# Kernel optimization log

Measured on AMD Instinct MI355X. Metric: run time of the kernel, lower is better.

## Reference

```python
import jax, jax.numpy as jnp
import numpy as np

N = 50000      # nodes
E = 800000     # edges
D = 128        # input_dim = nb_hidden = emb_dim
A = 4          # nb_edge_types (edge attr dim)
H = 2          # heads (MyGATConv default)
G = 128        # number of graphs (g.batch)
NEG = 0.2      # leaky_relu negative slope
L = 3          # nb_layers


def _glorot(key, shape):
    lim = np.sqrt(6.0 / (shape[-2] + shape[-1]))
    return jax.random.uniform(key, shape, minval=-lim, maxval=lim, dtype=jnp.float32)


def setup_inputs():
    key = jax.random.key(0)
    ks = jax.random.split(key, 20)
    inp = {
        "x": jax.random.normal(ks[0], (N, D), jnp.float32),
        "edge_index": jax.random.randint(ks[1], (2, E), 0, N, dtype=jnp.int32),
        "edge_attr": jax.random.normal(ks[2], (E, A), jnp.float32),
        "batch": jnp.sort(jax.random.randint(ks[3], (N,), 0, G, dtype=jnp.int32)),
    }
    for l in range(L):
        inp[f"linN{l}"] = _glorot(ks[4 + 4 * l], (D, H * D))
        inp[f"linE{l}"] = _glorot(ks[5 + 4 * l], (A, H * A))
        inp[f"att{l}"] = _glorot(ks[6 + 4 * l], (1, H, 2 * D + A))
        inp[f"bias{l}"] = jnp.zeros((H * D,), jnp.float32)
    inp["fw"] = _glorot(ks[16], (D, 1))
    inp["fb"] = jnp.zeros((1,), jnp.float32)
    return inp


def _gat_layer(x_in, e_in, src, dst, linN, linE, att, bias):
    n = x_in.shape[0]
    x = (x_in @ linN + bias).reshape(n, H, D)              # [N,H,D]
    e = (e_in @ linE).reshape(-1, H, A)                    # [E,H,A]
    # alpha = (cat([x_i, x_j, e], -1) * att).sum(-1); x_i = x[src], x_j = x[dst]
    ai = jnp.einsum('nhc,hc->nh', x, att[0, :, :D])        # per-node, gathered at src
    aj = jnp.einsum('nhc,hc->nh', x, att[0, :, D:2 * D])   # per-node, gathered at dst
    ae = jnp.einsum('ehc,hc->eh', e, att[0, :, 2 * D:])
    alpha = jax.nn.leaky_relu(ai[src] + aj[dst] + ae, NEG)  # [E,H]
    # segment softmax over targets (edge_index[1])
    amax = jax.ops.segment_max(alpha, dst, num_segments=n)
    ex = jnp.exp(alpha - amax[dst])
    denom = jax.ops.segment_sum(ex, dst, num_segments=n)
    alpha = ex / denom[dst]
    # PyG propagate: message = alpha * x[src], scatter-add at dst
    msg = alpha[:, :, None] * x[src]                       # [E,H,D]
    out = jax.ops.segment_sum(msg, dst, num_segments=n) + x
    # concat=False -> mean over heads, then ReLU
    return jax.nn.relu(out.mean(axis=1)), jax.nn.relu(e.mean(axis=1))


def reference(x, edge_index, edge_attr, batch,
              linN0, linE0, att0, bias0,
              linN1, linE1, att1, bias1,
              linN2, linE2, att2, bias2,
              fw, fb):
    src, dst = edge_index[0], edge_index[1]
    params = [(linN0, linE0, att0, bias0),
              (linN1, linE1, att1, bias1),
              (linN2, linE2, att2, bias2)]
    h, e = x, edge_attr
    for (lN, lE, at, b) in params:
        h, e = _gat_layer(h, e, src, dst, lN, lE, at, b)
    pooled = jax.ops.segment_sum(h, batch, num_segments=G)  # global_add_pool -> [G,D]
    y = (pooled @ fw + fb).squeeze(-1)                      # [G]
    return y
```

## Files before the change

### kernel.cpp

```cpp
#include <hip/hip_runtime.h>
#include <hip/hip_bf16.h>

#define DD 128
#define AA 4
#define HH 2

typedef short short8 __attribute__((ext_vector_type(8)));
typedef float f32x4 __attribute__((ext_vector_type(4)));

__device__ inline unsigned short f2bf(float f) {
    unsigned u = __float_as_uint(f);
    unsigned r = (u + 0x7fffu + ((u >> 16) & 1u)) >> 16;
    return (unsigned short)r;
}
__device__ inline float4 unpack_bf16x4(uint2 v) {
    float4 r;
    r.x = __uint_as_float(v.x << 16);
    r.y = __uint_as_float(v.x & 0xffff0000u);
    r.z = __uint_as_float(v.y << 16);
    r.w = __uint_as_float(v.y & 0xffff0000u);
    return r;
}
__device__ inline uint2 pack_bf16x4(float a, float b, float c, float d) {
    uint2 p;
    p.x = (unsigned)f2bf(a) | ((unsigned)f2bf(b) << 16);
    p.y = (unsigned)f2bf(c) | ((unsigned)f2bf(d) << 16);
    return p;
}


__global__ void hist_kernel(const int* __restrict__ dst, int* __restrict__ cnt, int E) {
    int e = blockIdx.x * blockDim.x + threadIdx.x;
    if (e < E) atomicAdd(&cnt[dst[e]], 1);
}

__global__ __launch_bounds__(256) void scan1(const int* __restrict__ cnt,
                                             int* __restrict__ bsum, int N) {
    __shared__ int wsh[4];
    int b = blockIdx.x, t = threadIdx.x;
    int lane = t & 63, w = t >> 6;
    int base = b * 1024;
    int v = 0;
    #pragma unroll
    for (int i = 0; i < 4; ++i) {
        int idx = base + i * 256 + t;
        v += (idx < N) ? cnt[idx] : 0;
    }
    #pragma unroll
    for (int o = 32; o; o >>= 1) v += __shfl_xor(v, o);
    if (lane == 0) wsh[w] = v;
    __syncthreads();
    if (t == 0) bsum[b] = wsh[0] + wsh[1] + wsh[2] + wsh[3];
}

__global__ __launch_bounds__(64) void scan2(int* __restrict__ bsum, int NB,
                                            int* __restrict__ total) {
    int t = threadIdx.x;
    int v = (t < NB) ? bsum[t] : 0;
    int x = v;
    #pragma unroll
    for (int o = 1; o < 64; o <<= 1) {
        int u = __shfl_up(x, o);
        if (t >= o) x += u;
    }
    if (t < NB) bsum[t] = x - v;
    if (t == 63) *total = x;
}

__global__ __launch_bounds__(256) void scan3(const int* __restrict__ cnt,
                                             const int* __restrict__ bsum,
                                             int* __restrict__ row_off,
                                             int* __restrict__ cursor, int N) {
    __shared__ int wtot[4];
    __shared__ int carry;
    int b = blockIdx.x, t = threadIdx.x;
    int lane = t & 63, w = t >> 6;
    if (t == 0) carry = bsum[b];
    __syncthreads();
    int base = b * 1024;
    #pragma unroll
    for (int it = 0; it < 4; ++it) {
        int idx = base + it * 256 + t;
        int v = (idx < N) ? cnt[idx] : 0;
        int x = v;
        #pragma unroll
        for (int o = 1; o < 64; o <<= 1) {
            int u = __shfl_up(x, o);
            if (lane >= o) x += u;
        }
        if (lane == 63) wtot[w] = x;
        __syncthreads();
        int woff = 0;
        for (int i = 0; i < w; ++i) woff += wtot[i];
        int c = carry;
        __syncthreads();
        if (t == 255) carry = c + woff + x;
        int ex = c + woff + x - v;
        if (idx < N) { row_off[idx] = ex; cursor[idx] = ex; }
        __syncthreads();
    }
}

__global__ void scatter_kernel(const int* __restrict__ src, const int* __restrict__ dst,
                               int* __restrict__ cursor, int* __restrict__ csr_src,
                               int* __restrict__ pos_of_edge, int E) {
    int e = blockIdx.x * blockDim.x + threadIdx.x;
    if (e >= E) return;
    int p = atomicAdd(&cursor[dst[e]], 1);
    csr_src[p] = src[e];
    pos_of_edge[e] = p;
}


__global__ __launch_bounds__(256) void pack_a0(const float* __restrict__ X,
                                               uint2* __restrict__ As, int N) {
    int t = blockIdx.x * blockDim.x + threadIdx.x;
    if (t >= N * 32) return;
    int r = t >> 5, kq4 = t & 31;
    float4 v = ((const float4*)X)[t];
    int g = r >> 4, m = r & 15;
    int ks = kq4 >> 3, q = (kq4 >> 1) & 3;
    int cell = ((g * 4 + ks) * 4 + q) * 16 + m;
    As[cell * 2 + (kq4 & 1)] = pack_bf16x4(v.x, v.y, v.z, v.w);
}

__global__ __launch_bounds__(256) void pack_w3(const float* __restrict__ W0,
                                               const float* __restrict__ W1,
                                               const float* __restrict__ W2,
                                               unsigned short* __restrict__ Bs) {
    int t = blockIdx.x * blockDim.x + threadIdx.x;
    if (t >= 3 * 128 * 64) return;
    int l = t / (128 * 64);
    int r = t - l * (128 * 64);
    const float* W = (l == 0) ? W0 : (l == 1) ? W1 : W2;
    unsigned short* B = Bs + (size_t)l * 128 * 256;
    int k = r >> 6, c4g = r & 63;
    float4 v = ((const float4*)W)[r];
    int ct = c4g >> 2, n0 = (c4g & 3) * 4;
    int ks = k >> 5, q = (k >> 3) & 3, j = k & 7;
    int cellbase = ((ct * 4 + ks) * 4 + q) * 16 + n0;
    B[(cellbase + 0) * 8 + j] = f2bf(v.x);
    B[(cellbase + 1) * 8 + j] = f2bf(v.y);
    B[(cellbase + 2) * 8 + j] = f2bf(v.z);
    B[(cellbase + 3) * 8 + j] = f2bf(v.w);
}


__global__ __launch_bounds__(256) void gemm_mfma(const short8* __restrict__ As,
                                                 const short8* __restrict__ Bs,
                                                 const float* __restrict__ bias,
                                                 const float* __restrict__ att,
                                                 uint2* __restrict__ xhb,
                                                 float* __restrict__ aiaj, int Ngroups) {
    __shared__ __align__(16) unsigned short sh[4][16 * 260];
    int w = threadIdx.x >> 6;
    int wid = blockIdx.x * 4 + w;
    int lane = threadIdx.x & 63;
    bool active = wid < Ngroups;
    int q = lane >> 4, m = lane & 15;

    if (active) {
        const short8* Ag = As + (size_t)wid * 256;
        f32x4 acc[16];
        #pragma unroll
        for (int ct = 0; ct < 16; ++ct) acc[ct] = (f32x4){0.f, 0.f, 0.f, 0.f};

        #pragma unroll
        for (int ks = 0; ks < 4; ++ks) {
            short8 a = Ag[ks * 64 + lane];
            #pragma unroll
            for (int ct = 0; ct < 16; ++ct) {
                short8 b = Bs[ct * 256 + ks * 64 + lane];
                acc[ct] = __builtin_amdgcn_mfma_f32_16x16x32_bf16(a, b, acc[ct], 0, 0, 0);
            }
        }

        float ai0[4] = {}, ai1[4] = {}, aj0[4] = {}, aj1[4] = {};
        #pragma unroll
        for (int ct = 0; ct < 16; ++ct) {
            int cbase = (ct & 7) * 16 + m;
            const float* atth = att + (ct >= 8 ? (2 * DD + AA) : 0);
            float aS = atth[cbase];
            float aD = atth[DD + cbase];
            float bv = bias[ct * 16 + m];
            #pragma unroll
            for (int reg = 0; reg < 4; ++reg) {
                float val = acc[ct][reg] + bv;
                sh[w][(q * 4 + reg) * 260 + ct * 16 + m] = f2bf(val);
                if (ct < 8) { ai0[reg] += val * aS; aj0[reg] += val * aD; }
                else        { ai1[reg] += val * aS; aj1[reg] += val * aD; }
            }
        }
        #pragma unroll
        for (int o = 1; o < 16; o <<= 1) {
            #pragma unroll
            for (int reg = 0; reg < 4; ++reg) {
                ai0[reg] += __shfl_xor(ai0[reg], o);
                ai1[reg] += __shfl_xor(ai1[reg], o);
                aj0[reg] += __shfl_xor(aj0[reg], o);
                aj1[reg] += __shfl_xor(aj1[reg], o);
            }
        }
        if (m == 0) {
            #pragma unroll
            for (int reg = 0; reg < 4; ++reg) {
                float4 r;
                r.x = ai0[reg]; r.y = ai1[reg]; r.z = aj0[reg]; r.w = aj1[reg];
                ((float4*)aiaj)[wid * 16 + q * 4 + reg] = r;
            }
        }
    }
    __syncthreads();
    if (active) {
        #pragma unroll
        for (int lr = 0; lr < 16; ++lr) {
            uint2 v = *(const uint2*)&sh[w][lr * 260 + lane * 4];
            xhb[(size_t)(wid * 16 + lr) * 64 + lane] = v;
        }
    }
}


__device__ inline void edge_stage(const float4& ev, const float* __restrict__ linE,
                                  const float* __restrict__ att, float2& ae, float4& enext) {
    float eh[8];
    #pragma unroll
    for (int c = 0; c < 8; ++c)
        eh[c] = ev.x * linE[c] + ev.y * linE[8 + c] + ev.z * linE[16 + c] + ev.w * linE[24 + c];
    float a0 = 0.f, a1 = 0.f;
    #pragma unroll
    for (int a = 0; a < 4; ++a) {
        a0 += eh[a]     * att[2 * DD + a];
        a1 += eh[4 + a] * att[(2 * DD + AA) + 2 * DD + a];
    }
    ae.x = a0; ae.y = a1;
    enext.x = fmaxf(0.5f * (eh[0] + eh[4]), 0.f);
    enext.y = fmaxf(0.5f * (eh[1] + eh[5]), 0.f);
    enext.z = fmaxf(0.5f * (eh[2] + eh[6]), 0.f);
    enext.w = fmaxf(0.5f * (eh[3] + eh[7]), 0.f);
}

__global__ __launch_bounds__(256) void edge_all(const float* __restrict__ ein,
                                                const float* __restrict__ linE0, const float* __restrict__ att0,
                                                const float* __restrict__ linE1, const float* __restrict__ att1,
                                                const float* __restrict__ linE2, const float* __restrict__ att2,
                                                const int* __restrict__ pos_of_edge,
                                                float2* __restrict__ ae0,
                                                float2* __restrict__ ae1,
                                                float2* __restrict__ ae2, int E) {
    int e = blockIdx.x * blockDim.x + threadIdx.x;
    if (e >= E) return;
    int p = pos_of_edge[e];
    float4 ev = ((const float4*)ein)[e];
    float2 ae; float4 en;
    edge_stage(ev, linE0, att0, ae, en); ae0[p] = ae;
    edge_stage(en, linE1, att1, ae, ev); ae1[p] = ae;
    edge_stage(ev, linE2, att2, ae, en); ae2[p] = ae;
}


__global__ __launch_bounds__(64) void aggregate(const uint2* __restrict__ xhb,
                                                const float* __restrict__ aiaj,
                                                const float2* __restrict__ ae,
                                                const int* __restrict__ row_off,
                                                const int* __restrict__ csr_src,
                                                uint2* __restrict__ hshuf,
                                                const float* __restrict__ fw,
                                                float* __restrict__ pdots, int N) {
    int d = blockIdx.x;
    int lane = threadIdx.x;
    int s0 = row_off[d], s1 = row_off[d + 1];
    int deg = s1 - s0;
    const float2* aiaj2 = (const float2*)aiaj;
    float2 ajv = aiaj2[d * 2 + 1];

    __shared__ float lex[64][2];
    __shared__ int lsrc[64];
    float4 acc = {0.f, 0.f, 0.f, 0.f};
    float den0 = 0.f, den1 = 0.f;
    int head = lane >> 5;

    for (int c = 0; c < deg; c += 64) {
        int n = min(64, deg - c);
        if (lane < n) {
            int p = s0 + c + lane;
            int s = csr_src[p];
            float2 aiv = aiaj2[s * 2];
            float2 aev = ae[p];
            float a0 = aiv.x + ajv.x + aev.x; a0 = a0 > 0.f ? a0 : 0.2f * a0;
            float a1 = aiv.y + ajv.y + aev.y; a1 = a1 > 0.f ? a1 : 0.2f * a1;
            float e0 = __expf(a0), e1 = __expf(a1);
            den0 += e0; den1 += e1;
            lex[lane][0] = e0; lex[lane][1] = e1;
            lsrc[lane] = s;
        }
        __syncthreads();
        #pragma unroll 4
        for (int j = 0; j < n; ++j) {
            float wgt = lex[j][head];
            float4 xv = unpack_bf16x4(xhb[(size_t)lsrc[j] * 64 + lane]);
            acc.x += wgt * xv.x; acc.y += wgt * xv.y;
            acc.z += wgt * xv.z; acc.w += wgt * xv.w;
        }
        __syncthreads();
    }

    #pragma unroll
    for (int o = 32; o; o >>= 1) {
        den0 += __shfl_xor(den0, o);
        den1 += __shfl_xor(den1, o);
    }
    float den = head ? den1 : den0;
    if (deg == 0) den = 1.0f;
    float inv = 1.0f / den;

    float4 xd = unpack_bf16x4(xhb[(size_t)d * 64 + lane]);
    float4 v;
    v.x = acc.x * inv + xd.x;
    v.y = acc.y * inv + xd.y;
    v.z = acc.z * inv + xd.z;
    v.w = acc.w * inv + xd.w;
    float4 o2;
    o2.x = __shfl_xor(v.x, 32);
    o2.y = __shfl_xor(v.y, 32);
    o2.z = __shfl_xor(v.z, 32);
    o2.w = __shfl_xor(v.w, 32);
    if (lane < 32) {
        float4 r;
        r.x = fmaxf(0.5f * (v.x + o2.x), 0.f);
        r.y = fmaxf(0.5f * (v.y + o2.y), 0.f);
        r.z = fmaxf(0.5f * (v.z + o2.z), 0.f);
        r.w = fmaxf(0.5f * (v.w + o2.w), 0.f);
        if (hshuf) {
            int g = d >> 4, m = d & 15;
            int ks = lane >> 3, q = (lane >> 1) & 3;
            int cell = ((g * 4 + ks) * 4 + q) * 16 + m;
            hshuf[cell * 2 + (lane & 1)] = pack_bf16x4(r.x, r.y, r.z, r.w);
        }
        if (pdots) {
            float4 wv = ((const float4*)fw)[lane];
            float pd = r.x * wv.x + r.y * wv.y + r.z * wv.z + r.w * wv.w;
            #pragma unroll
            for (int o = 16; o; o >>= 1) pd += __shfl_xor(pd, o);
            if (lane == 0) pdots[d] = pd;
        }
    }
}


__global__ __launch_bounds__(256) void segpool_kernel(const float* __restrict__ p,
                                                      const int* __restrict__ batch,
                                                      float* __restrict__ y, int N, int G) {
    __shared__ float bins[128];
    int t = threadIdx.x;
    if (t < G) bins[t] = 0.f;
    __syncthreads();
    int per = (N + gridDim.x - 1) / gridDim.x;
    int lo = blockIdx.x * per;
    int hi = min(lo + per, N);
    float acc = 0.f;
    int key = -1;
    for (int i = lo + t; i < hi; i += 256) {
        int k = batch[i];
        float v = p[i];
        if (k != key) {
            if (key >= 0) atomicAdd(&bins[key], acc);
            key = k;
            acc = 0.f;
        }
        acc += v;
    }
    if (key >= 0) atomicAdd(&bins[key], acc);
    __syncthreads();
    if (t < G && bins[t] != 0.f) atomicAdd(&y[t], bins[t]);
}

__global__ void init_y(float* __restrict__ y, const float* __restrict__ fb, int G) {
    int g = blockIdx.x * blockDim.x + threadIdx.x;
    if (g < G) y[g] = fb[0];
}


extern "C" void kernel_launch(void* const* d_in, const int* in_sizes, int n_in,
                              void* d_out, int out_size, void* d_ws, size_t ws_size,
                              hipStream_t stream) {
    const float* x     = (const float*)d_in[0];
    const int*   ei    = (const int*)d_in[1];
    const float* eattr = (const float*)d_in[2];
    const int*   batch = (const int*)d_in[3];
    const float* fw    = (const float*)d_in[16];
    const float* fb    = (const float*)d_in[17];
    float* y = (float*)d_out;

    const int N = in_sizes[0] / DD;
    const int E = in_sizes[1] / 2;
    const int G = out_size;

    const int* src = ei;
    const int* dst = ei + E;

    char* ws = (char*)d_ws;
    size_t off = 0;
    auto carve = [&](size_t bytes) {
        char* p = ws + off;
        off += (bytes + 255) & ~(size_t)255;
        return p;
    };
    uint2*  xhb     = (uint2*)carve((size_t)N * 256 * 2);
    uint2*  S0      = (uint2*)carve((size_t)N * 128 * 2);
    uint2*  S1      = (uint2*)carve((size_t)N * 128 * 2);
    unsigned short* Bs = (unsigned short*)carve((size_t)3 * 128 * 256 * 2);
    float2* ae0     = (float2*)carve((size_t)E * 2 * 4);
    float2* ae1     = (float2*)carve((size_t)E * 2 * 4);
    float2* ae2     = (float2*)carve((size_t)E * 2 * 4);
    float*  aiaj    = (float*)carve((size_t)N * 4 * 4);
    int*    row_off = (int*)carve((size_t)(N + 1) * 4);
    int*    cursor  = (int*)carve((size_t)N * 4);
    int*    cnt     = (int*)carve((size_t)N * 4);
    int*    csr_src = (int*)carve((size_t)E * 4);
    int*    pos     = (int*)carve((size_t)E * 4);
    float*  pdots   = (float*)carve((size_t)N * 4);
    int*    bsum    = (int*)carve((size_t)256 * 4);

    const int NB = (N + 1023) / 1024;
    const int Ngroups = N / 16;

    hipMemsetAsync(cnt, 0, (size_t)N * 4, stream);
    int eb = (E + 255) / 256;
    hist_kernel<<<eb, 256, 0, stream>>>(dst, cnt, E);
    scan1<<<NB, 256, 0, stream>>>(cnt, bsum, N);
    scan2<<<1, 64, 0, stream>>>(bsum, NB, row_off + N);
    scan3<<<NB, 256, 0, stream>>>(cnt, bsum, row_off, cursor, N);
    scatter_kernel<<<eb, 256, 0, stream>>>(src, dst, cursor, csr_src, pos, E);

    edge_all<<<eb, 256, 0, stream>>>(eattr,
                                     (const float*)d_in[5], (const float*)d_in[6],
                                     (const float*)d_in[9], (const float*)d_in[10],
                                     (const float*)d_in[13], (const float*)d_in[14],
                                     pos, ae0, ae1, ae2, E);

    pack_a0<<<(N * 32 + 255) / 256, 256, 0, stream>>>(x, S0, N);
    pack_w3<<<(3 * 128 * 64 + 255) / 256, 256, 0, stream>>>(
        (const float*)d_in[4], (const float*)d_in[8], (const float*)d_in[12], Bs);

    int gemm_blocks = (Ngroups + 3) / 4;
    float2* aes[3] = {ae0, ae1, ae2};
    uint2* Ain[3]  = {S0, S1, S0};
    uint2* Aout[3] = {S1, S0, nullptr};

    for (int l = 0; l < 3; ++l) {
        const float* att  = (const float*)d_in[6 + 4 * l];
        const float* bias = (const float*)d_in[7 + 4 * l];
        const short8* Bl  = (const short8*)(Bs + (size_t)l * 128 * 256);

        gemm_mfma<<<gemm_blocks, 256, 0, stream>>>((const short8*)Ain[l], Bl,
                                                   bias, att, xhb, aiaj, Ngroups);
        aggregate<<<N, 64, 0, stream>>>(xhb, aiaj, aes[l], row_off, csr_src,
                                        Aout[l], fw, (l == 2) ? pdots : nullptr, N);
    }

    init_y<<<1, 128, 0, stream>>>(y, fb, G);
    segpool_kernel<<<128, 256, 0, stream>>>(pdots, batch, y, N, G);
}
```

Baseline: 521.1 us.

## Split GEMM per head across waves, gather edges via CSR ids, fold init_y

The GEMM now gives each wave one head's half of the output columns for a 16-row group. This halves the accumulator registers and doubles the wave count, and the block-wide barrier becomes per-wave work. The scatter now stores the original edge id per CSR slot, so edge_all does coalesced writes and gathered reads instead of scattered writes. The init_y launch is folded into scan1, and barriers in the single-wave aggregate loop are dropped. That barrier removal relies on wave-synchronous execution of the 64-thread block for the shared-memory reads to be correct.

```diff
diff --git a/kernel.cpp b/kernel.cpp
--- a/kernel.cpp
+++ b/kernel.cpp
@@ -35,10 +35,13 @@
 }
 
 __global__ __launch_bounds__(256) void scan1(const int* __restrict__ cnt,
-                                             int* __restrict__ bsum, int N) {
+                                             int* __restrict__ bsum, int N,
+                                             float* __restrict__ y,
+                                             const float* __restrict__ fb) {
     __shared__ int wsh[4];
     int b = blockIdx.x, t = threadIdx.x;
     int lane = t & 63, w = t >> 6;
+    if (b == 0 && t < 128) y[t] = fb[0];
     int base = b * 1024;
     int v = 0;
     #pragma unroll
@@ -103,12 +106,12 @@
 
 __global__ void scatter_kernel(const int* __restrict__ src, const int* __restrict__ dst,
                                int* __restrict__ cursor, int* __restrict__ csr_src,
-                               int* __restrict__ pos_of_edge, int E) {
+                               int* __restrict__ csr_eid, int E) {
     int e = blockIdx.x * blockDim.x + threadIdx.x;
     if (e >= E) return;
     int p = atomicAdd(&cursor[dst[e]], 1);
     csr_src[p] = src[e];
-    pos_of_edge[e] = p;
+    csr_eid[p] = e;
 }
 
 
@@ -152,71 +155,66 @@
                                                  const float* __restrict__ att,
                                                  uint2* __restrict__ xhb,
                                                  float* __restrict__ aiaj, int Ngroups) {
-    __shared__ __align__(16) unsigned short sh[4][16 * 260];
+    __shared__ __align__(16) unsigned short sh[4][16 * 132];
     int w = threadIdx.x >> 6;
-    int wid = blockIdx.x * 4 + w;
+    int flat = blockIdx.x * 4 + w;
+    int wid = flat >> 1, half = flat & 1;
     int lane = threadIdx.x & 63;
-    bool active = wid < Ngroups;
+    if (wid >= Ngroups) return;
     int q = lane >> 4, m = lane & 15;
 
-    if (active) {
-        const short8* Ag = As + (size_t)wid * 256;
-        f32x4 acc[16];
+    const short8* Ag = As + (size_t)wid * 256;
+    f32x4 acc[8];
+    #pragma unroll
+    for (int c8 = 0; c8 < 8; ++c8) acc[c8] = (f32x4){0.f, 0.f, 0.f, 0.f};
+
+    #pragma unroll
+    for (int ks = 0; ks < 4; ++ks) {
+        short8 a = Ag[ks * 64 + lane];
         #pragma unroll
-        for (int ct = 0; ct < 16; ++ct) acc[ct] = (f32x4){0.f, 0.f, 0.f, 0.f};
-
+        for (int c8 = 0; c8 < 8; ++c8) {
+            short8 b = Bs[(half * 8 + c8) * 256 + ks * 64 + lane];
+            acc[c8] = __builtin_amdgcn_mfma_f32_16x16x32_bf16(a, b, acc[c8], 0, 0, 0);
+        }
+    }
+
+    const float* atth = att + half * (2 * DD + AA);
+    float ai[4] = {}, aj[4] = {};
+    #pragma unroll
+    for (int c8 = 0; c8 < 8; ++c8) {
+        int col = c8 * 16 + m;
+        float aS = atth[col];
+        float aD = atth[DD + col];
+        float bv = bias[(half * 8 + c8) * 16 + m];
         #pragma unroll
-        for (int ks = 0; ks < 4; ++ks) {
-            short8 a = Ag[ks * 64 + lane];
-            #pragma unroll
-            for (int ct = 0; ct < 16; ++ct) {
-                short8 b = Bs[ct * 256 + ks * 64 + lane];
-                acc[ct] = __builtin_amdgcn_mfma_f32_16x16x32_bf16(a, b, acc[ct], 0, 0, 0);
-            }
-        }
-
-        float ai0[4] = {}, ai1[4] = {}, aj0[4] = {}, aj1[4] = {};
+        for (int reg = 0; reg < 4; ++reg) {
+            float val = acc[c8][reg] + bv;
+            sh[w][(q * 4 + reg) * 132 + col] = f2bf(val);
+            ai[reg] += val * aS;
+            aj[reg] += val * aD;
+        }
+    }
+    #pragma unroll
+    for (int o = 1; o < 16; o <<= 1) {
         #pragma unroll
-        for (int ct = 0; ct < 16; ++ct) {
-            int cbase = (ct & 7) * 16 + m;
-            const float* atth = att + (ct >= 8 ? (2 * DD + AA) : 0);
-            float aS = atth[cbase];
-            float aD = atth[DD + cbase];
-            float bv = bias[ct * 16 + m];
-            #pragma unroll
-            for (int reg = 0; reg < 4; ++reg) {
-                float val = acc[ct][reg] + bv;
-                sh[w][(q * 4 + reg) * 260 + ct * 16 + m] = f2bf(val);
-                if (ct < 8) { ai0[reg] += val * aS; aj0[reg] += val * aD; }
-                else        { ai1[reg] += val * aS; aj1[reg] += val * aD; }
-            }
-        }
+        for (int reg = 0; reg < 4; ++reg) {
+            ai[reg] += __shfl_xor(ai[reg], o);
+            aj[reg] += __shfl_xor(aj[reg], o);
+        }
+    }
+    if (m == 0) {
         #pragma unroll
-        for (int o = 1; o < 16; o <<= 1) {
-            #pragma unroll
-            for (int reg = 0; reg < 4; ++reg) {
-                ai0[reg] += __shfl_xor(ai0[reg], o);
-                ai1[reg] += __shfl_xor(ai1[reg], o);
-                aj0[reg] += __shfl_xor(aj0[reg], o);
-                aj1[reg] += __shfl_xor(aj1[reg], o);
-            }
-        }
-        if (m == 0) {
-            #pragma unroll
-            for (int reg = 0; reg < 4; ++reg) {
-                float4 r;
-                r.x = ai0[reg]; r.y = ai1[reg]; r.z = aj0[reg]; r.w = aj1[reg];
-                ((float4*)aiaj)[wid * 16 + q * 4 + reg] = r;
-            }
-        }
-    }
-    __syncthreads();
-    if (active) {
-        #pragma unroll
-        for (int lr = 0; lr < 16; ++lr) {
-            uint2 v = *(const uint2*)&sh[w][lr * 260 + lane * 4];
-            xhb[(size_t)(wid * 16 + lr) * 64 + lane] = v;
-        }
+        for (int reg = 0; reg < 4; ++reg) {
+            int row = wid * 16 + q * 4 + reg;
+            aiaj[row * 4 + half] = ai[reg];
+            aiaj[row * 4 + 2 + half] = aj[reg];
+        }
+    }
+    #pragma unroll
+    for (int r2 = 0; r2 < 8; ++r2) {
+        int row = r2 * 2 + (lane >> 5);
+        uint2 v = *(const uint2*)&sh[w][row * 132 + (lane & 31) * 4];
+        xhb[(size_t)(wid * 16 + row) * 64 + half * 32 + (lane & 31)] = v;
     }
 }
 
@@ -244,14 +242,14 @@
                                                 const float* __restrict__ linE0, const float* __restrict__ att0,
                                                 const float* __restrict__ linE1, const float* __restrict__ att1,
                                                 const float* __restrict__ linE2, const float* __restrict__ att2,
-                                                const int* __restrict__ pos_of_edge,
+                                                const int* __restrict__ csr_eid,
                                                 float2* __restrict__ ae0,
                                                 float2* __restrict__ ae1,
                                                 float2* __restrict__ ae2, int E) {
-    int e = blockIdx.x * blockDim.x + threadIdx.x;
-    if (e >= E) return;
-    int p = pos_of_edge[e];
-    float4 ev = ((const float4*)ein)[e];
+    int p = blockIdx.x * blockDim.x + threadIdx.x;
+    if (p >= E) return;
+    int eid = csr_eid[p];
+    float4 ev = ((const float4*)ein)[eid];
     float2 ae; float4 en;
     edge_stage(ev, linE0, att0, ae, en); ae0[p] = ae;
     edge_stage(en, linE1, att1, ae, ev); ae1[p] = ae;
@@ -294,7 +292,6 @@
             lex[lane][0] = e0; lex[lane][1] = e1;
             lsrc[lane] = s;
         }
-        __syncthreads();
         #pragma unroll 4
         for (int j = 0; j < n; ++j) {
             float wgt = lex[j][head];
@@ -302,7 +299,6 @@
             acc.x += wgt * xv.x; acc.y += wgt * xv.y;
             acc.z += wgt * xv.z; acc.w += wgt * xv.w;
         }
-        __syncthreads();
     }
 
     #pragma unroll
@@ -375,11 +371,6 @@
     if (t < G && bins[t] != 0.f) atomicAdd(&y[t], bins[t]);
 }
 
-__global__ void init_y(float* __restrict__ y, const float* __restrict__ fb, int G) {
-    int g = blockIdx.x * blockDim.x + threadIdx.x;
-    if (g < G) y[g] = fb[0];
-}
-
 
 extern "C" void kernel_launch(void* const* d_in, const int* in_sizes, int n_in,
                               void* d_out, int out_size, void* d_ws, size_t ws_size,
@@ -418,7 +409,7 @@
     int*    cursor  = (int*)carve((size_t)N * 4);
     int*    cnt     = (int*)carve((size_t)N * 4);
     int*    csr_src = (int*)carve((size_t)E * 4);
-    int*    pos     = (int*)carve((size_t)E * 4);
+    int*    csr_eid = (int*)carve((size_t)E * 4);
     float*  pdots   = (float*)carve((size_t)N * 4);
     int*    bsum    = (int*)carve((size_t)256 * 4);
 
@@ -428,22 +419,22 @@
     hipMemsetAsync(cnt, 0, (size_t)N * 4, stream);
     int eb = (E + 255) / 256;
     hist_kernel<<<eb, 256, 0, stream>>>(dst, cnt, E);
-    scan1<<<NB, 256, 0, stream>>>(cnt, bsum, N);
+    scan1<<<NB, 256, 0, stream>>>(cnt, bsum, N, y, fb);
     scan2<<<1, 64, 0, stream>>>(bsum, NB, row_off + N);
     scan3<<<NB, 256, 0, stream>>>(cnt, bsum, row_off, cursor, N);
-    scatter_kernel<<<eb, 256, 0, stream>>>(src, dst, cursor, csr_src, pos, E);
+    scatter_kernel<<<eb, 256, 0, stream>>>(src, dst, cursor, csr_src, csr_eid, E);
 
     edge_all<<<eb, 256, 0, stream>>>(eattr,
                                      (const float*)d_in[5], (const float*)d_in[6],
                                      (const float*)d_in[9], (const float*)d_in[10],
                                      (const float*)d_in[13], (const float*)d_in[14],
-                                     pos, ae0, ae1, ae2, E);
+                                     csr_eid, ae0, ae1, ae2, E);
 
     pack_a0<<<(N * 32 + 255) / 256, 256, 0, stream>>>(x, S0, N);
     pack_w3<<<(3 * 128 * 64 + 255) / 256, 256, 0, stream>>>(
         (const float*)d_in[4], (const float*)d_in[8], (const float*)d_in[12], Bs);
 
-    int gemm_blocks = (Ngroups + 3) / 4;
+    int gemm_blocks = (Ngroups * 2 + 3) / 4;
     float2* aes[3] = {ae0, ae1, ae2};
     uint2* Ain[3]  = {S0, S1, S0};
     uint2* Aout[3] = {S1, S0, nullptr};
@@ -459,6 +450,5 @@
                                         Aout[l], fw, (l == 2) ? pdots : nullptr, N);
     }
 
-    init_y<<<1, 128, 0, stream>>>(y, fb, G);
     segpool_kernel<<<128, 256, 0, stream>>>(pdots, batch, y, N, G);
 }
```

Measured after the change: 477.3 us. -8.4%, faster.
